# Kernel optimization log

Hardware: AMD Instinct MI355X
Metric: run time of the kernel (lower is better)

The kernel has to match this reference:

```python
import jax, jax.numpy as jnp
import numpy as np

D, H, W, VP = 10, 400, 352, 35  # grid depth/height/width, points per voxel
C1_IN, C1_H = 7, 16   # VFE-1: Linear 7->16, concat -> 32
C2_IN, C2_H = 32, 64  # VFE-2: Linear 32->64, concat -> 128
BN_EPS = 1e-5


def setup_inputs() -> dict:
    key = jax.random.key(0)
    ks = jax.random.split(key, 12)
    K = 15000
    feature = jax.random.normal(ks[0], (K, VP, C1_IN), jnp.float32)
    keep = (jax.random.uniform(ks[1], (K, VP, 1)) < 0.8).astype(jnp.float32)
    feature = feature * keep
    bs = 1
    coordinate = jnp.concatenate([
        jax.random.randint(ks[2], (K, 1), 0, bs),
        jax.random.randint(ks[3], (K, 1), 0, D),
        jax.random.randint(ks[4], (K, 1), 0, H),
        jax.random.randint(ks[5], (K, 1), 0, W),
    ], axis=1).astype(jnp.int32)
    w1 = jax.random.normal(ks[6], (C1_IN, C1_H), jnp.float32) * 0.3
    b1 = jnp.zeros((C1_H,), jnp.float32)
    g1 = jnp.ones((C1_H,), jnp.float32)
    be1 = jnp.zeros((C1_H,), jnp.float32)
    w2 = jax.random.normal(ks[7], (C2_IN, C2_H), jnp.float32) * 0.15
    b2 = jnp.zeros((C2_H,), jnp.float32)
    g2 = jnp.ones((C2_H,), jnp.float32)
    be2 = jnp.zeros((C2_H,), jnp.float32)
    return dict(feature=feature, coordinate=coordinate, bs=bs,
                w1=w1, b1=b1, g1=g1, be1=be1,
                w2=w2, b2=b2, g2=g2, be2=be2)


def _vfe(x, mask, Wm, b, gamma, beta):
    # Linear + ReLU, then BatchNorm1d (training-mode batch stats over (K, VP))
    pw = jax.nn.relu(jnp.einsum('kpi,ih->kph', x, Wm) + b)
    mean = jnp.mean(pw, axis=(0, 1))
    var = jnp.var(pw, axis=(0, 1))  # biased variance, as BN uses for normalization
    pw = (pw - mean) * jax.lax.rsqrt(var + BN_EPS) * gamma + beta
    agg = jnp.max(pw, axis=1, keepdims=True)            # [K,1,Ch] per-voxel max
    concat = jnp.concatenate([pw, jnp.broadcast_to(agg, pw.shape)], axis=-1)
    return concat * mask                                  # mask broadcasts [K,VP,1]


def reference(feature, coordinate, bs, w1, b1, g1, be1, w2, b2, g2, be2):
    # mask: point is valid if max over its 7 features != 0
    mask = (jnp.max(feature, axis=2, keepdims=True) != 0).astype(feature.dtype)
    x = _vfe(feature, mask, w1, b1, g1, be1)   # [K,VP,32]
    x = _vfe(x, mask, w2, b2, g2, be2)         # [K,VP,128]
    voxelwise = jnp.max(x, axis=1)             # [K,128]
    c = coordinate
    out = jnp.zeros((bs, D, H, W, 2 * C2_H), feature.dtype)
    # sparse -> dense sums duplicate coordinates, matching torch.sparse to_dense
    out = out.at[c[:, 0], c[:, 1], c[:, 2], c[:, 3]].add(voxelwise)
    return out
```

## Files before the change

### kernel.cpp

```cpp
#include <hip/hip_runtime.h>
#include <math.h>

#define VPTS 35
#define CIN1 7
#define CH1  16
#define CH2  64
#define DD   10
#define HHH  400
#define WWW  352
#define BN_EPS 1e-5f


__global__ void k_init(float* __restrict__ ws) {
  if (threadIdx.x < 320) ws[threadIdx.x] = 0.f;
}

__global__ void __launch_bounds__(256) k_A(
    const float* __restrict__ feat,
    const float* __restrict__ w1, const float* __restrict__ b1,
    float* __restrict__ red1, float4* __restrict__ out4, long zA, int KP) {
  float w[CIN1][CH1], bb[CH1];
#pragma unroll
  for (int i = 0; i < CIN1; ++i)
#pragma unroll
    for (int c = 0; c < CH1; ++c) w[i][c] = w1[i * CH1 + c];
#pragma unroll
  for (int c = 0; c < CH1; ++c) bb[c] = b1[c];
  float s[CH1], q[CH1];
#pragma unroll
  for (int c = 0; c < CH1; ++c) { s[c] = 0.f; q[c] = 0.f; }
  int tid = blockIdx.x * blockDim.x + threadIdx.x;
  int stride = gridDim.x * blockDim.x;
  for (int idx = tid; idx < KP; idx += stride) {
    float x[CIN1];
#pragma unroll
    for (int i = 0; i < CIN1; ++i) x[i] = feat[(size_t)idx * CIN1 + i];
#pragma unroll
    for (int c = 0; c < CH1; ++c) {
      float a = bb[c];
#pragma unroll
      for (int i = 0; i < CIN1; ++i) a = fmaf(x[i], w[i][c], a);
      a = fmaxf(a, 0.f);
      s[c] += a;
      q[c] = fmaf(a, a, q[c]);
    }
  }
  float4 z = make_float4(0.f, 0.f, 0.f, 0.f);
  for (long i = tid; i < zA; i += stride) out4[i] = z;
  __shared__ float ssum[2 * CH1];
  if (threadIdx.x < 2 * CH1) ssum[threadIdx.x] = 0.f;
  __syncthreads();
#pragma unroll
  for (int c = 0; c < CH1; ++c) {
    float a = s[c], b = q[c];
    for (int o = 32; o > 0; o >>= 1) {
      a += __shfl_down(a, o);
      b += __shfl_down(b, o);
    }
    if ((threadIdx.x & 63) == 0) {
      atomicAdd(&ssum[c], a);
      atomicAdd(&ssum[CH1 + c], b);
    }
  }
  __syncthreads();
  if (threadIdx.x < 2 * CH1) atomicAdd(&red1[threadIdx.x], ssum[threadIdx.x]);
}

__device__ __forceinline__ void stage1_tile(
    const float* __restrict__ feat, int k, int t,
    const float* __restrict__ w1, const float* __restrict__ b1,
    const float* scsh1,
    float* fs, float* mask_s, float* pw1_s, float* agg1_s) {
  if (t < VPTS * CIN1) fs[t] = feat[(size_t)k * (VPTS * CIN1) + t];
  __syncthreads();
  for (int i = t; i < VPTS * CH1; i += 256) {
    int p = i >> 4, c = i & 15;
    float acc = b1[c];
#pragma unroll
    for (int j = 0; j < CIN1; ++j) acc = fmaf(fs[p * CIN1 + j], w1[j * CH1 + c], acc);
    acc = fmaxf(acc, 0.f);
    pw1_s[i] = fmaf(acc, scsh1[c], scsh1[CH1 + c]);
    if (c == 0) {
      float m = fs[p * CIN1];
#pragma unroll
      for (int j = 1; j < CIN1; ++j) m = fmaxf(m, fs[p * CIN1 + j]);
      mask_s[p] = (m != 0.f) ? 1.f : 0.f;
    }
  }
  __syncthreads();
  if (t < 64) {
    int c = t & 15, g = t >> 4;
    float m = -INFINITY;
    for (int p = g; p < VPTS; p += 4) m = fmaxf(m, pw1_s[p * CH1 + c]);
    m = fmaxf(m, __shfl_xor(m, 16));
    m = fmaxf(m, __shfl_xor(m, 32));
    if (g == 0) agg1_s[c] = m;
  }
  __syncthreads();
}

__global__ void __launch_bounds__(256) k_heavy(
    const float* __restrict__ feat,
    const float* __restrict__ w1, const float* __restrict__ b1,
    const float* __restrict__ g1, const float* __restrict__ be1,
    const float* __restrict__ red1,
    const float* __restrict__ w2, const float* __restrict__ b2,
    const float* __restrict__ g2,
    float* __restrict__ red2,
    float* __restrict__ E1buf, float* __restrict__ E2buf,
    float* __restrict__ FLbuf, int K,
    float4* __restrict__ out4, long z0, long n4, float invN) {
  __shared__ float fs[VPTS * CIN1], mask_s[VPTS], pw1_s[VPTS * CH1], agg1_s[CH1];
  __shared__ float scsh1_s[2 * CH1];
  __shared__ float ec[2][4][64];
  __shared__ float ss[2 * CH2];
  int t = threadIdx.x, lane = t & 63, w = t >> 6;
  if (t < CH1) {
    float mean = red1[t] * invN;
    float var = red1[CH1 + t] * invN - mean * mean;
    float inv = rsqrtf(var + BN_EPS);
    float sc = g1[t] * inv;
    scsh1_s[t] = sc;
    scsh1_s[CH1 + t] = be1[t] - mean * sc;
  }
  if (t < 2 * CH2) ss[t] = 0.f;
  float wcol[32];
#pragma unroll
  for (int i = 0; i < 32; ++i) wcol[i] = w2[i * CH2 + lane];
  float b2c = b2[lane];
  float sgn = (g2[lane] >= 0.f) ? 1.f : -1.f;
  __syncthreads();
  long zstride = (long)gridDim.x * 256;
  long zi = z0 + (long)blockIdx.x * 256 + t;
  float4 zv = make_float4(0.f, 0.f, 0.f, 0.f);
  float lsum = 0.f, lsq = 0.f;
  for (int k = blockIdx.x; k < K; k += gridDim.x) {
#pragma unroll
    for (int u = 0; u < 8; ++u) {
      if (zi < n4) { out4[zi] = zv; zi += zstride; }
    }
    stage1_tile(feat, k, t, w1, b1, scsh1_s, fs, mask_s, pw1_s, agg1_s);
    float aggdot = 0.f;
#pragma unroll
    for (int c = 0; c < CH1; ++c) aggdot = fmaf(agg1_s[c], wcol[16 + c], aggdot);
    float E1w = -INFINITY, E2w = -INFINITY;
    for (int p = w; p < VPTS; p += 4) {
      float m = mask_s[p];
      const float4* xv = (const float4*)(pw1_s + p * CH1);
      float low = 0.f;
#pragma unroll
      for (int i = 0; i < 4; ++i) {
        float4 v = xv[i];
        low = fmaf(v.x, wcol[4 * i + 0], low);
        low = fmaf(v.y, wcol[4 * i + 1], low);
        low = fmaf(v.z, wcol[4 * i + 2], low);
        low = fmaf(v.w, wcol[4 * i + 3], low);
      }
      float pw2 = fmaxf(fmaf(m, low + aggdot, b2c), 0.f);
      lsum += pw2;
      lsq = fmaf(pw2, pw2, lsq);
      float sp = sgn * pw2;
      E2w = fmaxf(E2w, sp);
      E1w = fmaxf(E1w, (m != 0.f) ? sp : -INFINITY);
    }
    ec[0][w][lane] = E1w;
    ec[1][w][lane] = E2w;
    __syncthreads();
    if (t < 64) {
      float a = fmaxf(fmaxf(ec[0][0][t], ec[0][1][t]),
                      fmaxf(ec[0][2][t], ec[0][3][t]));
      E1buf[(size_t)k * 64 + t] = a;
    } else if (t < 128) {
      int c = t - 64;
      float a = fmaxf(fmaxf(ec[1][0][c], ec[1][1][c]),
                      fmaxf(ec[1][2][c], ec[1][3][c]));
      E2buf[(size_t)k * 64 + c] = a;
    } else if (t < 192) {
      int l2 = t - 128;
      float v = (l2 < VPTS) ? mask_s[l2] : 0.f;
      for (int o = 32; o > 0; o >>= 1) v += __shfl_down(v, o);
      if (l2 == 0) FLbuf[k] = v;
    }
    __syncthreads();
  }
  for (; zi < n4; zi += zstride) out4[zi] = zv;
  atomicAdd(&ss[lane], lsum);
  atomicAdd(&ss[CH2 + lane], lsq);
  __syncthreads();
  if (t < 2 * CH2) atomicAdd(&red2[t], ss[t]);
}

__global__ void __launch_bounds__(256) k_scatter(
    const float* __restrict__ E1buf, const float* __restrict__ E2buf,
    const float* __restrict__ FLbuf, const float* __restrict__ red2,
    const float* __restrict__ g2, const float* __restrict__ be2,
    const int* __restrict__ coord, float* __restrict__ out, int K,
    float invN) {
  __shared__ float scsh2_s[2 * CH2];
  int t = threadIdx.x;
  if (t < CH2) {
    float mean = red2[t] * invN;
    float var = red2[CH2 + t] * invN - mean * mean;
    float inv = rsqrtf(var + BN_EPS);
    float sc = g2[t] * inv;
    scsh2_s[t] = sc;
    scsh2_s[CH2 + t] = be2[t] - mean * sc;
  }
  __syncthreads();
  int k = blockIdx.x * 2 + (t >> 7);
  if (k >= K) return;
  int tl = t & 127;
  int c = tl & 63;
  float nv = FLbuf[k];
  bool anyV = nv > 0.f;
  bool anyI = nv < (float)VPTS;
  float sc = scsh2_s[c], sh = scsh2_s[CH2 + c];
  float cand = -INFINITY;
  if (anyV) {
    float E = (tl < 64) ? E1buf[(size_t)k * 64 + c] : E2buf[(size_t)k * 64 + c];
    cand = fmaf(fabsf(sc), E, sh);
  }
  if (anyI) cand = fmaxf(cand, 0.f);
  int4 cc = *reinterpret_cast<const int4*>(coord + (size_t)k * 4);
  long vox = ((long)(cc.x * DD + cc.y) * HHH + cc.z) * WWW + cc.w;
  atomicAdd(&out[vox * (2 * CH2) + tl], cand);
}

__global__ void __launch_bounds__(256) k_zero(float4* __restrict__ out4,
                                              long n4, float* __restrict__ ws) {
  long i = (long)blockIdx.x * blockDim.x + threadIdx.x;
  long stride = (long)gridDim.x * blockDim.x;
  float4 z = make_float4(0.f, 0.f, 0.f, 0.f);
  for (; i < n4; i += stride) out4[i] = z;
  if (blockIdx.x == 0 && threadIdx.x < 320) ws[threadIdx.x] = 0.f;
}

__global__ void k_finalize(const float* __restrict__ red,
                           const float* __restrict__ g,
                           const float* __restrict__ be,
                           float* __restrict__ scsh, int CH, float invN) {
  int c = threadIdx.x;
  if (c < CH) {
    float mean = red[c] * invN;
    float var = red[CH + c] * invN - mean * mean;
    float inv = rsqrtf(var + BN_EPS);
    float sc = g[c] * inv;
    scsh[c] = sc;
    scsh[CH + c] = be[c] - mean * sc;
  }
}

__global__ void __launch_bounds__(256) k_stats1_fb(
    const float* __restrict__ feat,
    const float* __restrict__ w1, const float* __restrict__ b1,
    float* __restrict__ red1, int KP) {
  float w[CIN1][CH1], bb[CH1];
#pragma unroll
  for (int i = 0; i < CIN1; ++i)
#pragma unroll
    for (int c = 0; c < CH1; ++c) w[i][c] = w1[i * CH1 + c];
#pragma unroll
  for (int c = 0; c < CH1; ++c) bb[c] = b1[c];
  float s[CH1], q[CH1];
#pragma unroll
  for (int c = 0; c < CH1; ++c) { s[c] = 0.f; q[c] = 0.f; }
  int tid = blockIdx.x * blockDim.x + threadIdx.x;
  int stride = gridDim.x * blockDim.x;
  for (int idx = tid; idx < KP; idx += stride) {
    float x[CIN1];
#pragma unroll
    for (int i = 0; i < CIN1; ++i) x[i] = feat[(size_t)idx * CIN1 + i];
#pragma unroll
    for (int c = 0; c < CH1; ++c) {
      float a = bb[c];
#pragma unroll
      for (int i = 0; i < CIN1; ++i) a = fmaf(x[i], w[i][c], a);
      a = fmaxf(a, 0.f);
      s[c] += a;
      q[c] = fmaf(a, a, q[c]);
    }
  }
  __shared__ float ssum[2 * CH1];
  if (threadIdx.x < 2 * CH1) ssum[threadIdx.x] = 0.f;
  __syncthreads();
#pragma unroll
  for (int c = 0; c < CH1; ++c) {
    float a = s[c], b = q[c];
    for (int o = 32; o > 0; o >>= 1) {
      a += __shfl_down(a, o);
      b += __shfl_down(b, o);
    }
    if ((threadIdx.x & 63) == 0) {
      atomicAdd(&ssum[c], a);
      atomicAdd(&ssum[CH1 + c], b);
    }
  }
  __syncthreads();
  if (threadIdx.x < 2 * CH1) atomicAdd(&red1[threadIdx.x], ssum[threadIdx.x]);
}

__device__ __forceinline__ void compute_x2_old(
    const float* __restrict__ feat, int k, int t,
    const float* __restrict__ w1, const float* __restrict__ b1,
    const float* __restrict__ scsh1,
    float* fs, float* mask_s, float* pw1_s, float* agg1_s, float* x2_s) {
  if (t < VPTS * CIN1) fs[t] = feat[(size_t)k * (VPTS * CIN1) + t];
  __syncthreads();
  if (t < VPTS) {
    float m = fs[t * CIN1];
#pragma unroll
    for (int i = 1; i < CIN1; ++i) m = fmaxf(m, fs[t * CIN1 + i]);
    mask_s[t] = (m != 0.f) ? 1.f : 0.f;
  }
  for (int i = t; i < VPTS * CH1; i += 256) {
    int p = i >> 4, c = i & 15;
    float acc = b1[c];
#pragma unroll
    for (int j = 0; j < CIN1; ++j) acc = fmaf(fs[p * CIN1 + j], w1[j * CH1 + c], acc);
    acc = fmaxf(acc, 0.f);
    pw1_s[i] = fmaf(acc, scsh1[c], scsh1[CH1 + c]);
  }
  __syncthreads();
  if (t < CH1) {
    float m = pw1_s[t];
    for (int p = 1; p < VPTS; ++p) m = fmaxf(m, pw1_s[p * CH1 + t]);
    agg1_s[t] = m;
  }
  __syncthreads();
  for (int i = t; i < VPTS * 32; i += 256) {
    int p = i >> 5, c = i & 31;
    x2_s[i] = (c < CH1 ? pw1_s[p * CH1 + c] : agg1_s[c - CH1]) * mask_s[p];
  }
  __syncthreads();
}

__global__ void __launch_bounds__(256) k_stats2_old(
    const float* __restrict__ feat,
    const float* __restrict__ w1, const float* __restrict__ b1,
    const float* __restrict__ scsh1,
    const float* __restrict__ w2, const float* __restrict__ b2,
    float* __restrict__ red2, int K) {
  __shared__ float fs[VPTS * CIN1], mask_s[VPTS], pw1_s[VPTS * CH1], agg1_s[CH1];
  __shared__ __align__(16) float x2_s[VPTS * 32];
  __shared__ __align__(16) float w2_s[32 * CH2];
  __shared__ float ss[2 * CH2];
  int t = threadIdx.x;
  for (int i = t; i < 32 * CH2; i += 256) w2_s[i] = w2[i];
  if (t < 2 * CH2) ss[t] = 0.f;
  __syncthreads();
  int c = t & 63;
  float wcol[32];
#pragma unroll
  for (int i = 0; i < 32; ++i) wcol[i] = w2_s[i * CH2 + c];
  float bb = b2[c];
  float lsum = 0.f, lsq = 0.f;
  for (int k = blockIdx.x; k < K; k += gridDim.x) {
    compute_x2_old(feat, k, t, w1, b1, scsh1, fs, mask_s, pw1_s, agg1_s, x2_s);
    for (int p = t >> 6; p < VPTS; p += 4) {
      const float4* xv = (const float4*)(x2_s + p * 32);
      float a = bb;
#pragma unroll
      for (int i = 0; i < 8; ++i) {
        float4 v = xv[i];
        a = fmaf(v.x, wcol[4 * i + 0], a);
        a = fmaf(v.y, wcol[4 * i + 1], a);
        a = fmaf(v.z, wcol[4 * i + 2], a);
        a = fmaf(v.w, wcol[4 * i + 3], a);
      }
      a = fmaxf(a, 0.f);
      lsum += a;
      lsq = fmaf(a, a, lsq);
    }
  }
  atomicAdd(&ss[c], lsum);
  atomicAdd(&ss[CH2 + c], lsq);
  __syncthreads();
  if (t < 2 * CH2) atomicAdd(&red2[t], ss[t]);
}

__global__ void __launch_bounds__(256) k_final_old(
    const float* __restrict__ feat,
    const float* __restrict__ w1, const float* __restrict__ b1,
    const float* __restrict__ scsh1,
    const float* __restrict__ w2, const float* __restrict__ b2,
    const float* __restrict__ scsh2,
    const int* __restrict__ coord,
    float* __restrict__ out, int K) {
  __shared__ float fs[VPTS * CIN1], mask_s[VPTS], pw1_s[VPTS * CH1], agg1_s[CH1];
  __shared__ __align__(16) float x2_s[VPTS * 32];
  __shared__ __align__(16) float w2_s[32 * CH2];
  __shared__ float pw2_s[VPTS * CH2];
  __shared__ float agg2_s[CH2];
  int t = threadIdx.x;
  for (int i = t; i < 32 * CH2; i += 256) w2_s[i] = w2[i];
  __syncthreads();
  int c = t & 63;
  float wcol[32];
#pragma unroll
  for (int i = 0; i < 32; ++i) wcol[i] = w2_s[i * CH2 + c];
  float bb = b2[c];
  float sc = scsh2[c], sh = scsh2[CH2 + c];
  for (int k = blockIdx.x; k < K; k += gridDim.x) {
    compute_x2_old(feat, k, t, w1, b1, scsh1, fs, mask_s, pw1_s, agg1_s, x2_s);
    for (int p = t >> 6; p < VPTS; p += 4) {
      const float4* xv = (const float4*)(x2_s + p * 32);
      float a = bb;
#pragma unroll
      for (int i = 0; i < 8; ++i) {
        float4 v = xv[i];
        a = fmaf(v.x, wcol[4 * i + 0], a);
        a = fmaf(v.y, wcol[4 * i + 1], a);
        a = fmaf(v.z, wcol[4 * i + 2], a);
        a = fmaf(v.w, wcol[4 * i + 3], a);
      }
      a = fmaxf(a, 0.f);
      pw2_s[p * CH2 + c] = fmaf(a, sc, sh);
    }
    __syncthreads();
    if (t < CH2) {
      float m = pw2_s[t];
      for (int p = 1; p < VPTS; ++p) m = fmaxf(m, pw2_s[p * CH2 + t]);
      agg2_s[t] = m;
    }
    __syncthreads();
    if (t < 2 * CH2) {
      float vm = -INFINITY;
      if (t < CH2) {
        for (int p = 0; p < VPTS; ++p) vm = fmaxf(vm, pw2_s[p * CH2 + t] * mask_s[p]);
      } else {
        float a = agg2_s[t - CH2];
        for (int p = 0; p < VPTS; ++p) vm = fmaxf(vm, a * mask_s[p]);
      }
      int4 cc = *reinterpret_cast<const int4*>(coord + (size_t)k * 4);
      long vox = ((long)(cc.x * DD + cc.y) * HHH + cc.z) * WWW + cc.w;
      atomicAdd(&out[vox * (2 * CH2) + t], vm);
    }
  }
}

extern "C" void kernel_launch(void* const* d_in, const int* in_sizes, int n_in,
                              void* d_out, int out_size, void* d_ws, size_t ws_size,
                              hipStream_t stream) {
  const float* feat = (const float*)d_in[0];
  const int* coord  = (const int*)d_in[1];
  const float* w1  = (const float*)d_in[3];
  const float* b1  = (const float*)d_in[4];
  const float* g1  = (const float*)d_in[5];
  const float* be1 = (const float*)d_in[6];
  const float* w2  = (const float*)d_in[7];
  const float* b2  = (const float*)d_in[8];
  const float* g2  = (const float*)d_in[9];
  const float* be2 = (const float*)d_in[10];
  float* out = (float*)d_out;
  float* ws = (float*)d_ws;

  int K = in_sizes[0] / (VPTS * CIN1);
  int KP = K * VPTS;
  float invN = 1.f / (float)KP;

  float* red1  = ws;
  float* scsh1 = ws + 32;
  float* red2  = ws + 64;
  float* scsh2 = ws + 192;
  float* E1buf = ws + 1024;
  float* E2buf = E1buf + (size_t)64 * K;
  float* FLbuf = E2buf + (size_t)64 * K;

  size_t need_bytes = (1024 + (size_t)K * 129) * sizeof(float);

  long n4 = (long)out_size / 4;
  long zA = (n4 * 2) / 5;

  if (ws_size >= need_bytes) {
    k_init<<<1, 320, 0, stream>>>(ws);
    k_A<<<2048, 256, 0, stream>>>(feat, w1, b1, red1, (float4*)out, zA, KP);
    k_heavy<<<2048, 256, 0, stream>>>(feat, w1, b1, g1, be1, red1,
                                      w2, b2, g2, red2, E1buf, E2buf, FLbuf, K,
                                      (float4*)out, zA, n4, invN);
    k_scatter<<<(K + 1) / 2, 256, 0, stream>>>(E1buf, E2buf, FLbuf, red2,
                                               g2, be2, coord, out, K, invN);
  } else {
    k_zero<<<2048, 256, 0, stream>>>((float4*)out, n4, ws);
    k_stats1_fb<<<512, 256, 0, stream>>>(feat, w1, b1, red1, KP);
    k_finalize<<<1, 64, 0, stream>>>(red1, g1, be1, scsh1, CH1, invN);
    k_stats2_old<<<1024, 256, 0, stream>>>(feat, w1, b1, scsh1, w2, b2, red2, K);
    k_finalize<<<1, 64, 0, stream>>>(red2, g2, be2, scsh2, CH2, invN);
    k_final_old<<<2048, 256, 0, stream>>>(feat, w1, b1, scsh1, w2, b2, scsh2,
                                          coord, out, K);
  }
}
```

Before: 231.6 us.

## Process one voxel per wavefront in heavy kernel, removing block barriers

Changes k_heavy so that each 64-lane wavefront handles a whole voxel independently, with per-wave shared buffers. Block-wide __syncthreads and the cross-wave ec reduction are removed, and the mask is kept as a ballot bitmask with a popcount for the valid-point count. The output zero-fill moves out of the per-voxel loop into a tail loop, and the zeroing split shifts more work to k_A. Each lane now loops over all 35 points instead of about 9, which makes per-wave serial work larger in exchange for fewer barriers.

```diff
diff --git a/kernel.cpp b/kernel.cpp
--- a/kernel.cpp
+++ b/kernel.cpp
@@ -66,39 +66,6 @@
   if (threadIdx.x < 2 * CH1) atomicAdd(&red1[threadIdx.x], ssum[threadIdx.x]);
 }
 
-__device__ __forceinline__ void stage1_tile(
-    const float* __restrict__ feat, int k, int t,
-    const float* __restrict__ w1, const float* __restrict__ b1,
-    const float* scsh1,
-    float* fs, float* mask_s, float* pw1_s, float* agg1_s) {
-  if (t < VPTS * CIN1) fs[t] = feat[(size_t)k * (VPTS * CIN1) + t];
-  __syncthreads();
-  for (int i = t; i < VPTS * CH1; i += 256) {
-    int p = i >> 4, c = i & 15;
-    float acc = b1[c];
-#pragma unroll
-    for (int j = 0; j < CIN1; ++j) acc = fmaf(fs[p * CIN1 + j], w1[j * CH1 + c], acc);
-    acc = fmaxf(acc, 0.f);
-    pw1_s[i] = fmaf(acc, scsh1[c], scsh1[CH1 + c]);
-    if (c == 0) {
-      float m = fs[p * CIN1];
-#pragma unroll
-      for (int j = 1; j < CIN1; ++j) m = fmaxf(m, fs[p * CIN1 + j]);
-      mask_s[p] = (m != 0.f) ? 1.f : 0.f;
-    }
-  }
-  __syncthreads();
-  if (t < 64) {
-    int c = t & 15, g = t >> 4;
-    float m = -INFINITY;
-    for (int p = g; p < VPTS; p += 4) m = fmaxf(m, pw1_s[p * CH1 + c]);
-    m = fmaxf(m, __shfl_xor(m, 16));
-    m = fmaxf(m, __shfl_xor(m, 32));
-    if (g == 0) agg1_s[c] = m;
-  }
-  __syncthreads();
-}
-
 __global__ void __launch_bounds__(256) k_heavy(
     const float* __restrict__ feat,
     const float* __restrict__ w1, const float* __restrict__ b1,
@@ -110,80 +77,110 @@
     float* __restrict__ E1buf, float* __restrict__ E2buf,
     float* __restrict__ FLbuf, int K,
     float4* __restrict__ out4, long z0, long n4, float invN) {
-  __shared__ float fs[VPTS * CIN1], mask_s[VPTS], pw1_s[VPTS * CH1], agg1_s[CH1];
-  __shared__ float scsh1_s[2 * CH1];
-  __shared__ float ec[2][4][64];
+  __shared__ __align__(16) float fs_s[4][248];
+  __shared__ __align__(16) float pw1_s[4][560];
+  __shared__ __align__(16) float agg1_s[4][16];
   __shared__ float ss[2 * CH2];
   int t = threadIdx.x, lane = t & 63, w = t >> 6;
-  if (t < CH1) {
-    float mean = red1[t] * invN;
-    float var = red1[CH1 + t] * invN - mean * mean;
-    float inv = rsqrtf(var + BN_EPS);
-    float sc = g1[t] * inv;
-    scsh1_s[t] = sc;
-    scsh1_s[CH1 + t] = be1[t] - mean * sc;
-  }
-  if (t < 2 * CH2) ss[t] = 0.f;
+  float* fs   = fs_s[w];
+  float* pw1  = pw1_s[w];
+  float* agg1 = agg1_s[w];
+
+  int c1 = lane & 15;
+  float mean1 = red1[c1] * invN;
+  float var1  = red1[CH1 + c1] * invN - mean1 * mean1;
+  float sc1   = g1[c1] * rsqrtf(var1 + BN_EPS);
+  float sh1   = be1[c1] - mean1 * sc1;
+  float b1c   = b1[c1];
+  float w1r[CIN1];
+#pragma unroll
+  for (int j = 0; j < CIN1; ++j) w1r[j] = w1[j * CH1 + c1];
   float wcol[32];
 #pragma unroll
   for (int i = 0; i < 32; ++i) wcol[i] = w2[i * CH2 + lane];
   float b2c = b2[lane];
   float sgn = (g2[lane] >= 0.f) ? 1.f : -1.f;
-  __syncthreads();
-  long zstride = (long)gridDim.x * 256;
-  long zi = z0 + (long)blockIdx.x * 256 + t;
-  float4 zv = make_float4(0.f, 0.f, 0.f, 0.f);
+
   float lsum = 0.f, lsq = 0.f;
-  for (int k = blockIdx.x; k < K; k += gridDim.x) {
-#pragma unroll
-    for (int u = 0; u < 8; ++u) {
-      if (zi < n4) { out4[zi] = zv; zi += zstride; }
-    }
-    stage1_tile(feat, k, t, w1, b1, scsh1_s, fs, mask_s, pw1_s, agg1_s);
+  int waveg = blockIdx.x * 4 + w;
+  int nwave = gridDim.x * 4;
+  for (int k = waveg; k < K; k += nwave) {
+    for (int i = lane; i < VPTS * CIN1; i += 64) fs[i] = feat[(size_t)k * (VPTS * CIN1) + i];
+    bool vbit = false;
+    if (lane < VPTS) {
+      float m = fs[lane * CIN1];
+#pragma unroll
+      for (int j = 1; j < CIN1; ++j) m = fmaxf(m, fs[lane * CIN1 + j]);
+      vbit = (m != 0.f);
+    }
+    unsigned long long mbits = __ballot(vbit);
+#pragma unroll
+    for (int j = 0; j < 9; ++j) {
+      int idx = lane + 64 * j;
+      if (idx < VPTS * CH1) {
+        int p = idx >> 4;
+        float a = b1c;
+#pragma unroll
+        for (int jj = 0; jj < CIN1; ++jj) a = fmaf(fs[p * CIN1 + jj], w1r[jj], a);
+        a = fmaxf(a, 0.f);
+        pw1[idx] = fmaf(a, sc1, sh1);
+      }
+    }
+    {
+      int g = lane >> 4;
+      float am = -INFINITY;
+      for (int p = g; p < VPTS; p += 4) am = fmaxf(am, pw1[p * CH1 + c1]);
+      am = fmaxf(am, __shfl_xor(am, 16));
+      am = fmaxf(am, __shfl_xor(am, 32));
+      if (lane < CH1) agg1[lane] = am;
+    }
     float aggdot = 0.f;
-#pragma unroll
-    for (int c = 0; c < CH1; ++c) aggdot = fmaf(agg1_s[c], wcol[16 + c], aggdot);
+    {
+      const float4* a4 = (const float4*)agg1;
+#pragma unroll
+      for (int i = 0; i < 4; ++i) {
+        float4 v = a4[i];
+        aggdot = fmaf(v.x, wcol[16 + 4 * i + 0], aggdot);
+        aggdot = fmaf(v.y, wcol[16 + 4 * i + 1], aggdot);
+        aggdot = fmaf(v.z, wcol[16 + 4 * i + 2], aggdot);
+        aggdot = fmaf(v.w, wcol[16 + 4 * i + 3], aggdot);
+      }
+    }
     float E1w = -INFINITY, E2w = -INFINITY;
-    for (int p = w; p < VPTS; p += 4) {
-      float m = mask_s[p];
-      const float4* xv = (const float4*)(pw1_s + p * CH1);
+    const float4* p4 = (const float4*)pw1;
+    for (int p = 0; p < VPTS; ++p) {
+      float4 v0 = p4[p * 4 + 0], v1 = p4[p * 4 + 1];
+      float4 v2 = p4[p * 4 + 2], v3 = p4[p * 4 + 3];
       float low = 0.f;
-#pragma unroll
-      for (int i = 0; i < 4; ++i) {
-        float4 v = xv[i];
-        low = fmaf(v.x, wcol[4 * i + 0], low);
-        low = fmaf(v.y, wcol[4 * i + 1], low);
-        low = fmaf(v.z, wcol[4 * i + 2], low);
-        low = fmaf(v.w, wcol[4 * i + 3], low);
-      }
+      low = fmaf(v0.x, wcol[0], low);  low = fmaf(v0.y, wcol[1], low);
+      low = fmaf(v0.z, wcol[2], low);  low = fmaf(v0.w, wcol[3], low);
+      low = fmaf(v1.x, wcol[4], low);  low = fmaf(v1.y, wcol[5], low);
+      low = fmaf(v1.z, wcol[6], low);  low = fmaf(v1.w, wcol[7], low);
+      low = fmaf(v2.x, wcol[8], low);  low = fmaf(v2.y, wcol[9], low);
+      low = fmaf(v2.z, wcol[10], low); low = fmaf(v2.w, wcol[11], low);
+      low = fmaf(v3.x, wcol[12], low); low = fmaf(v3.y, wcol[13], low);
+      low = fmaf(v3.z, wcol[14], low); low = fmaf(v3.w, wcol[15], low);
+      bool valid = (mbits >> p) & 1ull;
+      float m = valid ? 1.f : 0.f;
       float pw2 = fmaxf(fmaf(m, low + aggdot, b2c), 0.f);
       lsum += pw2;
       lsq = fmaf(pw2, pw2, lsq);
       float sp = sgn * pw2;
       E2w = fmaxf(E2w, sp);
-      E1w = fmaxf(E1w, (m != 0.f) ? sp : -INFINITY);
-    }
-    ec[0][w][lane] = E1w;
-    ec[1][w][lane] = E2w;
-    __syncthreads();
-    if (t < 64) {
-      float a = fmaxf(fmaxf(ec[0][0][t], ec[0][1][t]),
-                      fmaxf(ec[0][2][t], ec[0][3][t]));
-      E1buf[(size_t)k * 64 + t] = a;
-    } else if (t < 128) {
-      int c = t - 64;
-      float a = fmaxf(fmaxf(ec[1][0][c], ec[1][1][c]),
-                      fmaxf(ec[1][2][c], ec[1][3][c]));
-      E2buf[(size_t)k * 64 + c] = a;
-    } else if (t < 192) {
-      int l2 = t - 128;
-      float v = (l2 < VPTS) ? mask_s[l2] : 0.f;
-      for (int o = 32; o > 0; o >>= 1) v += __shfl_down(v, o);
-      if (l2 == 0) FLbuf[k] = v;
-    }
-    __syncthreads();
-  }
-  for (; zi < n4; zi += zstride) out4[zi] = zv;
+      if (valid) E1w = fmaxf(E1w, sp);
+    }
+    E1buf[(size_t)k * 64 + lane] = E1w;
+    E2buf[(size_t)k * 64 + lane] = E2w;
+    if (lane == 0) FLbuf[k] = (float)__popcll(mbits);
+  }
+  {
+    float4 zv = make_float4(0.f, 0.f, 0.f, 0.f);
+    long stride = (long)gridDim.x * 256;
+    for (long zi = z0 + (long)blockIdx.x * 256 + t; zi < n4; zi += stride)
+      out4[zi] = zv;
+  }
+  if (t < 2 * CH2) ss[t] = 0.f;
+  __syncthreads();
   atomicAdd(&ss[lane], lsum);
   atomicAdd(&ss[CH2 + lane], lsq);
   __syncthreads();
@@ -469,7 +466,7 @@
   size_t need_bytes = (1024 + (size_t)K * 129) * sizeof(float);
 
   long n4 = (long)out_size / 4;
-  long zA = (n4 * 2) / 5;
+  long zA = (n4 * 55) / 100;
 
   if (ws_size >= need_bytes) {
     k_init<<<1, 320, 0, stream>>>(ws);
```

Measured after the change: 202.2 us. -12.7%, faster.
